# Kernel optimization log

Hardware: AMD Instinct MI355X
Metric: run time of the kernel (lower is better)

Reference implementation:

```python
import jax, jax.numpy as jnp
import numpy as np

N_NODES = 100000
N_EDGES = 1600000
N_FEAT = 64
HIDDEN = 64
N_GRAPHS = 256


def setup_inputs() -> dict:
    key = jax.random.key(0)
    ks = jax.random.split(key, 8)
    x = jax.random.normal(ks[0], (N_NODES, N_FEAT), dtype=jnp.float32)
    edge_index = jax.random.randint(ks[1], (2, N_EDGES), 0, N_NODES, dtype=jnp.int64)
    batch = jnp.sort(jax.random.randint(ks[2], (N_NODES,), 0, N_GRAPHS, dtype=jnp.int64))
    W1 = jax.random.normal(ks[3], (N_FEAT, HIDDEN), dtype=jnp.float32) / np.sqrt(N_FEAT)
    b1 = jnp.zeros((HIDDEN,), dtype=jnp.float32)
    W2 = jax.random.normal(ks[4], (HIDDEN, HIDDEN), dtype=jnp.float32) / np.sqrt(HIDDEN)
    b2 = jnp.zeros((HIDDEN,), dtype=jnp.float32)
    Wfc = jax.random.normal(ks[5], (HIDDEN, 1), dtype=jnp.float32) / np.sqrt(HIDDEN)
    bfc = jnp.zeros((1,), dtype=jnp.float32)
    return {"x": x, "edge_index": edge_index, "batch": batch,
            "W1": W1, "b1": b1, "W2": W2, "b2": b2, "Wfc": Wfc, "bfc": bfc}


def _gcn_conv(x, W, b, src, dst, norm, n_nodes):
    # h = X W, then symmetric-normalized scatter-add aggregation at dst
    h = x @ W  # [N, H]
    msg = h[src] * norm[:, None]  # [E+N, H] gather + scale
    agg = jax.ops.segment_sum(msg, dst, num_segments=n_nodes)
    return agg + b


def reference(x, edge_index, batch, W1, b1, W2, b2, Wfc, bfc):
    n = x.shape[0]
    loops = jnp.arange(n, dtype=edge_index.dtype)
    src = jnp.concatenate([edge_index[0], loops])  # add self-loops (GCNConv default)
    dst = jnp.concatenate([edge_index[1], loops])
    deg = jax.ops.segment_sum(jnp.ones_like(dst, dtype=x.dtype), dst, num_segments=n)
    dinv = jnp.where(deg > 0, jax.lax.rsqrt(deg), 0.0)
    norm = dinv[src] * dinv[dst]  # D^-1/2 (A+I) D^-1/2

    h = jax.nn.relu(_gcn_conv(x, W1, b1, src, dst, norm, n))  # dropout = identity (eval)
    h = jax.nn.relu(_gcn_conv(h, W2, b2, src, dst, norm, n))

    # global mean pool over graphs
    sums = jax.ops.segment_sum(h, batch, num_segments=N_GRAPHS)
    counts = jax.ops.segment_sum(jnp.ones((n,), dtype=h.dtype), batch, num_segments=N_GRAPHS)
    pooled = sums / jnp.maximum(counts, 1.0)[:, None]  # [G, H]
    return jax.nn.sigmoid(pooled @ Wfc + bfc)  # [G, 1]
```

## Files before the change

### kernel.cpp

```cpp
#include <hip/hip_runtime.h>
#include <hip/hip_fp16.h>
#include <math.h>

#define N_NODES  100000
#define N_EDGES  1600000
#define NF       64
#define N_GRAPHS 256

#define BSH   7
#define NB    ((N_NODES + 127) / 128)
#define BCAP  2600

typedef float f32x2 __attribute__((ext_vector_type(2)));

__global__ void k_zerocur(int* __restrict__ bucketCur) {
    int i = blockIdx.x * blockDim.x + threadIdx.x;
    if (i < NB) bucketCur[i] = 0;
}

__global__ __launch_bounds__(1024) void k_bscatter(const int* __restrict__ src,
                                                   const int* __restrict__ dst,
                                                   int* __restrict__ bucketCur,
                                                   int* __restrict__ scratch) {
    __shared__ int hist[NB];
    __shared__ int bbase[NB];
    int t = threadIdx.x;
    for (int i = t; i < NB; i += 1024) hist[i] = 0;
    __syncthreads();
    int e0 = (blockIdx.x * 1024 + t) * 8;
    int d[8], s[8], r[8];
    bool act = (e0 + 7) < N_EDGES;
    if (act) {
        *(int4*)&d[0] = *(const int4*)(dst + e0);
        *(int4*)&d[4] = *(const int4*)(dst + e0 + 4);
        *(int4*)&s[0] = *(const int4*)(src + e0);
        *(int4*)&s[4] = *(const int4*)(src + e0 + 4);
#pragma unroll
        for (int k = 0; k < 8; ++k) r[k] = atomicAdd(&hist[d[k] >> BSH], 1);
    }
    __syncthreads();
    for (int i = t; i < NB; i += 1024)
        if (hist[i]) bbase[i] = atomicAdd(&bucketCur[i], hist[i]);
    __syncthreads();
    if (act) {
#pragma unroll
        for (int k = 0; k < 8; ++k) {
            int b = d[k] >> BSH;
            int pos = bbase[b] + r[k];
            if (pos < BCAP)
                scratch[b * BCAP + pos] = ((d[k] & 127) << 17) | s[k];
        }
    }
}

__global__ __launch_bounds__(1024) void k_bscan(const int* __restrict__ bucketCur,
                                                int* __restrict__ bucketPtr,
                                                int* __restrict__ rowptr) {
    int t = threadIdx.x;
    __shared__ int ps[1024];
    int v = (t < NB) ? min(bucketCur[t], BCAP) : 0;
    ps[t] = v;
    __syncthreads();
#pragma unroll
    for (int off = 1; off < 1024; off <<= 1) {
        int u = (t >= off) ? ps[t - off] : 0;
        __syncthreads();
        ps[t] += u;
        __syncthreads();
    }
    if (t < NB) bucketPtr[t] = ps[t] - v;
    if (t == NB - 1) {
        bucketPtr[NB] = ps[t];
        rowptr[N_NODES] = ps[t];
    }
}

__global__ __launch_bounds__(256) void k_bfinal(const int* __restrict__ bucketCur,
                                                const int* __restrict__ bucketPtr,
                                                const int* __restrict__ scratch,
                                                int* __restrict__ rowptr,
                                                float* __restrict__ dinv,
                                                int* __restrict__ col) {
    int b = blockIdx.x;
    int cnt  = min(bucketCur[b], BCAP);
    int base = bucketPtr[b];
    int node0 = b << BSH;
    __shared__ int hist[128];
    __shared__ int escan[128];
    __shared__ int ps[128];
    __shared__ int rnk[BCAP];
    int t = threadIdx.x;
    if (t < 128) hist[t] = 0;
    __syncthreads();
    const int* sp = scratch + b * BCAP;
    for (int j = t; j < cnt; j += 256)
        rnk[j] = atomicAdd(&hist[sp[j] >> 17], 1);
    __syncthreads();
    int hv = (t < 128) ? hist[t] : 0;
    if (t < 128) ps[t] = hv;
    __syncthreads();
#pragma unroll
    for (int off = 1; off < 128; off <<= 1) {
        int u = 0;
        if (t < 128 && t >= off) u = ps[t - off];
        __syncthreads();
        if (t < 128) ps[t] += u;
        __syncthreads();
    }
    if (t < 128) {
        int excl = ps[t] - hv;
        escan[t] = excl;
        int node = node0 + t;
        if (node < N_NODES) {
            rowptr[node] = base + excl;
            dinv[node] = rsqrtf((float)(hv + 1));
        }
    }
    __syncthreads();
    for (int j = t; j < cnt; j += 256) {
        int pk = sp[j];
        col[base + escan[pk >> 17] + rnk[j]] = pk & 0x1FFFF;
    }
}

__global__ __launch_bounds__(256) void k_gemm(const float* __restrict__ X,
                                              const float* __restrict__ W,
                                              const float* __restrict__ bias,
                                              const float* __restrict__ dinv,
                                              int* __restrict__ Ah8) {
    __shared__ float Ws[64][64];
    __shared__ float Xs[64][68];
    int t  = threadIdx.x;
    int n0 = blockIdx.x * 64;

    for (int i = t; i < 64 * 64; i += 256) Ws[i >> 6][i & 63] = W[i];

#pragma unroll
    for (int p = 0; p < 4; ++p) {
        int flat = p * 256 + t;
        int nl = flat >> 4;
        int kg = flat & 15;
        int node = n0 + nl;
        float4 v = make_float4(0.f, 0.f, 0.f, 0.f);
        if (node < N_NODES) {
            v = *(const float4*)(X + (size_t)node * NF + kg * 4);
            if (bias) {
                v.x += bias[kg * 4 + 0]; v.x = v.x > 0.f ? v.x : 0.f;
                v.y += bias[kg * 4 + 1]; v.y = v.y > 0.f ? v.y : 0.f;
                v.z += bias[kg * 4 + 2]; v.z = v.z > 0.f ? v.z : 0.f;
                v.w += bias[kg * 4 + 3]; v.w = v.w > 0.f ? v.w : 0.f;
            }
        }
        Xs[kg * 4 + 0][nl] = v.x;
        Xs[kg * 4 + 1][nl] = v.y;
        Xs[kg * 4 + 2][nl] = v.z;
        Xs[kg * 4 + 3][nl] = v.w;
    }
    __syncthreads();

    int tx = t & 15;
    int ty = t >> 4;
    float acc[4][4];
#pragma unroll
    for (int i = 0; i < 4; ++i)
#pragma unroll
        for (int j = 0; j < 4; ++j) acc[i][j] = 0.f;

#pragma unroll 8
    for (int k = 0; k < 64; ++k) {
        float4 wv = *(const float4*)&Ws[k][tx * 4];
        float4 xv = *(const float4*)&Xs[k][ty * 4];
        acc[0][0] += xv.x * wv.x; acc[0][1] += xv.x * wv.y;
        acc[0][2] += xv.x * wv.z; acc[0][3] += xv.x * wv.w;
        acc[1][0] += xv.y * wv.x; acc[1][1] += xv.y * wv.y;
        acc[1][2] += xv.y * wv.z; acc[1][3] += xv.y * wv.w;
        acc[2][0] += xv.z * wv.x; acc[2][1] += xv.z * wv.y;
        acc[2][2] += xv.z * wv.z; acc[2][3] += xv.z * wv.w;
        acc[3][0] += xv.w * wv.x; acc[3][1] += xv.w * wv.y;
        acc[3][2] += xv.w * wv.z; acc[3][3] += xv.w * wv.w;
    }

#pragma unroll
    for (int i = 0; i < 4; ++i) {
        int node = n0 + ty * 4 + i;
        if (node < N_NODES) {
            float dv = dinv[node];
            int pk = 0;
            pk = __builtin_amdgcn_cvt_pk_fp8_f32(acc[i][0] * dv, acc[i][1] * dv, pk, false);
            pk = __builtin_amdgcn_cvt_pk_fp8_f32(acc[i][2] * dv, acc[i][3] * dv, pk, true);
            Ah8[(size_t)node * 16 + tx] = pk;
        }
    }
}

__global__ __launch_bounds__(256) void k_pull(const int* __restrict__ rowptr,
                                              const int* __restrict__ col,
                                              const float* __restrict__ dinv,
                                              const int* __restrict__ Ah8,
                                              float* __restrict__ B) {
    int n    = (blockIdx.x * blockDim.x + threadIdx.x) >> 6;
    int lane = threadIdx.x & 63;
    if (n >= N_NODES) return;
    int slot = lane >> 3;
    int oct  = lane & 7;
    int beg = rowptr[n];
    int cnt = rowptr[n + 1] - beg + 1;

    float acc0 = 0.f, acc1 = 0.f, acc2 = 0.f, acc3 = 0.f;
    float acc4 = 0.f, acc5 = 0.f, acc6 = 0.f, acc7 = 0.f;

    for (int base = slot; base < cnt; base += 32) {
        int cidx[4];
#pragma unroll
        for (int p = 0; p < 4; ++p) {
            int idx = base + p * 8;
            cidx[p] = (idx < cnt) ? ((idx == 0) ? n : col[beg + idx - 1]) : -1;
        }
#pragma unroll
        for (int p = 0; p < 4; ++p) {
            int s = cidx[p];
            if (s >= 0) {
                int2 raw = *(const int2*)(Ah8 + (size_t)s * 16 + oct * 2);
                f32x2 f0 = __builtin_amdgcn_cvt_pk_f32_fp8(raw.x, false);
                f32x2 f1 = __builtin_amdgcn_cvt_pk_f32_fp8(raw.x, true);
                f32x2 f2 = __builtin_amdgcn_cvt_pk_f32_fp8(raw.y, false);
                f32x2 f3 = __builtin_amdgcn_cvt_pk_f32_fp8(raw.y, true);
                acc0 += f0.x; acc1 += f0.y;
                acc2 += f1.x; acc3 += f1.y;
                acc4 += f2.x; acc5 += f2.y;
                acc6 += f3.x; acc7 += f3.y;
            }
        }
    }
#pragma unroll
    for (int off = 8; off < 64; off <<= 1) {
        acc0 += __shfl_down(acc0, off);
        acc1 += __shfl_down(acc1, off);
        acc2 += __shfl_down(acc2, off);
        acc3 += __shfl_down(acc3, off);
        acc4 += __shfl_down(acc4, off);
        acc5 += __shfl_down(acc5, off);
        acc6 += __shfl_down(acc6, off);
        acc7 += __shfl_down(acc7, off);
    }
    if (slot == 0) {
        float dv = dinv[n];
        float4 o0 = make_float4(acc0 * dv, acc1 * dv, acc2 * dv, acc3 * dv);
        float4 o1 = make_float4(acc4 * dv, acc5 * dv, acc6 * dv, acc7 * dv);
        *(float4*)(B + (size_t)n * NF + oct * 8)     = o0;
        *(float4*)(B + (size_t)n * NF + oct * 8 + 4) = o1;
    }
}

__device__ __forceinline__ int lower_bound_i(const int* __restrict__ a, int n, int key) {
    int lo = 0, hi = n;
    while (lo < hi) {
        int mid = (lo + hi) >> 1;
        if (a[mid] < key) lo = mid + 1; else hi = mid;
    }
    return lo;
}

__global__ __launch_bounds__(512) void k_pool_final(const float* __restrict__ B,
                                                    const int* __restrict__ batch,
                                                    const float* __restrict__ b2,
                                                    const float* __restrict__ Wfc,
                                                    const float* __restrict__ bfc,
                                                    float* __restrict__ out) {
    int g = blockIdx.x;
    __shared__ int s_lo, s_hi;
    int t = threadIdx.x;
    if (t == 0) {
        s_lo = lower_bound_i(batch, N_NODES, g);
        s_hi = lower_bound_i(batch, N_NODES, g + 1);
    }
    __syncthreads();
    int lo = s_lo, hi = s_hi;
    int ln = t >> 6, lane = t & 63;
    float bias = b2[lane];
    float acc = 0.0f;
    for (int n = lo + ln; n < hi; n += 8) {
        float v = B[(size_t)n * NF + lane] + bias;
        acc += v > 0.0f ? v : 0.0f;
    }
    __shared__ float red[8][64];
    red[ln][lane] = acc;
    __syncthreads();
    if (ln == 0) {
        float tot = 0.0f;
#pragma unroll
        for (int w = 0; w < 8; ++w) tot += red[w][lane];
        int cnt = hi - lo;
        float c = cnt > 0 ? (float)cnt : 1.0f;
        float v = (tot / c) * Wfc[lane];
#pragma unroll
        for (int off = 32; off > 0; off >>= 1) v += __shfl_down(v, off);
        if (lane == 0) out[g] = 1.0f / (1.0f + expf(-(v + bfc[0])));
    }
}

extern "C" void kernel_launch(void* const* d_in, const int* in_sizes, int n_in,
                              void* d_out, int out_size, void* d_ws, size_t ws_size,
                              hipStream_t stream) {
    const float* x    = (const float*)d_in[0];
    const int*   ei   = (const int*)d_in[1];
    const int*   batch= (const int*)d_in[2];
    const float* W1   = (const float*)d_in[3];
    const float* b1   = (const float*)d_in[4];
    const float* W2   = (const float*)d_in[5];
    const float* b2   = (const float*)d_in[6];
    const float* Wfc  = (const float*)d_in[7];
    const float* bfc  = (const float*)d_in[8];
    float* out = (float*)d_out;

    const int* src = ei;
    const int* dst = ei + N_EDGES;

    float*  B         = (float*)d_ws;
    int*    Ah8       = (int*)(B + (size_t)N_NODES * NF);
    float*  dinv      = (float*)(Ah8 + (size_t)N_NODES * 16);
    int*    rowptr    = (int*)(dinv + N_NODES);
    int*    bucketCur = rowptr + N_NODES + 1;
    int*    bucketPtr = bucketCur + NB;
    int*    col       = bucketPtr + NB + 1;
    int*    scratch   = col + N_EDGES;

    const int BLK = 256;
    int g_gemm  = (N_NODES + 63) / 64;
    int g_nwave = (N_NODES + 3) / 4;
    int g_bsc   = (N_EDGES / 8 + 1023) / 1024;

    k_zerocur<<<(NB + BLK - 1) / BLK, BLK, 0, stream>>>(bucketCur);
    k_bscatter<<<g_bsc, 1024, 0, stream>>>(src, dst, bucketCur, scratch);
    k_bscan<<<1, 1024, 0, stream>>>(bucketCur, bucketPtr, rowptr);
    k_bfinal<<<NB, BLK, 0, stream>>>(bucketCur, bucketPtr, scratch, rowptr, dinv, col);

    k_gemm<<<g_gemm, BLK, 0, stream>>>(x, W1, nullptr, dinv, Ah8);
    k_pull<<<g_nwave, BLK, 0, stream>>>(rowptr, col, dinv, Ah8, B);

    k_gemm<<<g_gemm, BLK, 0, stream>>>(B, W2, b1, dinv, Ah8);
    k_pull<<<g_nwave, BLK, 0, stream>>>(rowptr, col, dinv, Ah8, B);

    k_pool_final<<<N_GRAPHS, 512, 0, stream>>>(B, batch, b2, Wfc, bfc, out);
}
```

Baseline: 262.0 us.

## Fuse aggregation with GEMM and pooling, split fp8 features into halves

The layer-1 aggregation is fused into the layer-2 GEMM kernel and the layer-2 aggregation is fused with mean pooling, so the fp32 intermediate buffer B is never written or read. FP8 feature rows are split into two 32-byte half arrays, gathered in two passes with 16 edge slots per wave, to shrink the gather working set. Pooling accumulates per-block partial sums in shared memory and flushes them with global atomics. A small head kernel finishes the output. The cost is that each block now processes nodes one at a time per wave with a serial loop over 16 nodes and two passes. That may reduce parallelism and latency hiding compared with the previous one-wave-per-node pull.

```diff
diff --git a/kernel.cpp b/kernel.cpp
--- a/kernel.cpp
+++ b/kernel.cpp
@@ -1,5 +1,4 @@
 #include <hip/hip_runtime.h>
-#include <hip/hip_fp16.h>
 #include <math.h>
 
 #define N_NODES  100000
@@ -10,12 +9,14 @@
 #define BSH   7
 #define NB    ((N_NODES + 127) / 128)
 #define BCAP  2600
+#define NBLKS ((N_NODES + 63) / 64)
 
 typedef float f32x2 __attribute__((ext_vector_type(2)));
 
-__global__ void k_zerocur(int* __restrict__ bucketCur) {
+__global__ void k_zeroinit(int* __restrict__ bucketCur, float* __restrict__ gsums) {
     int i = blockIdx.x * blockDim.x + threadIdx.x;
     if (i < NB) bucketCur[i] = 0;
+    if (i < N_GRAPHS * NF) gsums[i] = 0.0f;
 }
 
 __global__ __launch_bounds__(1024) void k_bscatter(const int* __restrict__ src,
@@ -123,11 +124,11 @@
     }
 }
 
-__global__ __launch_bounds__(256) void k_gemm(const float* __restrict__ X,
-                                              const float* __restrict__ W,
-                                              const float* __restrict__ bias,
-                                              const float* __restrict__ dinv,
-                                              int* __restrict__ Ah8) {
+__global__ __launch_bounds__(256) void k_gemm1(const float* __restrict__ X,
+                                               const float* __restrict__ W,
+                                               const float* __restrict__ dinv,
+                                               int* __restrict__ A1a,
+                                               int* __restrict__ A1b) {
     __shared__ float Ws[64][64];
     __shared__ float Xs[64][68];
     int t  = threadIdx.x;
@@ -142,15 +143,7 @@
         int kg = flat & 15;
         int node = n0 + nl;
         float4 v = make_float4(0.f, 0.f, 0.f, 0.f);
-        if (node < N_NODES) {
-            v = *(const float4*)(X + (size_t)node * NF + kg * 4);
-            if (bias) {
-                v.x += bias[kg * 4 + 0]; v.x = v.x > 0.f ? v.x : 0.f;
-                v.y += bias[kg * 4 + 1]; v.y = v.y > 0.f ? v.y : 0.f;
-                v.z += bias[kg * 4 + 2]; v.z = v.z > 0.f ? v.z : 0.f;
-                v.w += bias[kg * 4 + 3]; v.w = v.w > 0.f ? v.w : 0.f;
-            }
-        }
+        if (node < N_NODES) v = *(const float4*)(X + (size_t)node * NF + kg * 4);
         Xs[kg * 4 + 0][nl] = v.x;
         Xs[kg * 4 + 1][nl] = v.y;
         Xs[kg * 4 + 2][nl] = v.z;
@@ -188,67 +181,170 @@
             int pk = 0;
             pk = __builtin_amdgcn_cvt_pk_fp8_f32(acc[i][0] * dv, acc[i][1] * dv, pk, false);
             pk = __builtin_amdgcn_cvt_pk_fp8_f32(acc[i][2] * dv, acc[i][3] * dv, pk, true);
-            Ah8[(size_t)node * 16 + tx] = pk;
-        }
-    }
-}
-
-__global__ __launch_bounds__(256) void k_pull(const int* __restrict__ rowptr,
-                                              const int* __restrict__ col,
-                                              const float* __restrict__ dinv,
-                                              const int* __restrict__ Ah8,
-                                              float* __restrict__ B) {
-    int n    = (blockIdx.x * blockDim.x + threadIdx.x) >> 6;
-    int lane = threadIdx.x & 63;
-    if (n >= N_NODES) return;
-    int slot = lane >> 3;
-    int oct  = lane & 7;
-    int beg = rowptr[n];
-    int cnt = rowptr[n + 1] - beg + 1;
-
-    float acc0 = 0.f, acc1 = 0.f, acc2 = 0.f, acc3 = 0.f;
-    float acc4 = 0.f, acc5 = 0.f, acc6 = 0.f, acc7 = 0.f;
-
-    for (int base = slot; base < cnt; base += 32) {
+            if (tx < 8) __builtin_nontemporal_store(pk, &A1a[(size_t)node * 8 + tx]);
+            else        __builtin_nontemporal_store(pk, &A1b[(size_t)node * 8 + tx - 8]);
+        }
+    }
+}
+
+__device__ __forceinline__ void pull_half(const int* __restrict__ A,
+                                          const int* __restrict__ col,
+                                          int n, int beg, int cnt,
+                                          int slot, int quad, float acc[8]) {
+#pragma unroll
+    for (int k = 0; k < 8; ++k) acc[k] = 0.f;
+    for (int base = slot; base < cnt; base += 64) {
         int cidx[4];
 #pragma unroll
         for (int p = 0; p < 4; ++p) {
-            int idx = base + p * 8;
+            int idx = base + p * 16;
             cidx[p] = (idx < cnt) ? ((idx == 0) ? n : col[beg + idx - 1]) : -1;
         }
 #pragma unroll
         for (int p = 0; p < 4; ++p) {
             int s = cidx[p];
             if (s >= 0) {
-                int2 raw = *(const int2*)(Ah8 + (size_t)s * 16 + oct * 2);
+                int2 raw = *(const int2*)(A + (size_t)s * 8 + quad * 2);
                 f32x2 f0 = __builtin_amdgcn_cvt_pk_f32_fp8(raw.x, false);
                 f32x2 f1 = __builtin_amdgcn_cvt_pk_f32_fp8(raw.x, true);
                 f32x2 f2 = __builtin_amdgcn_cvt_pk_f32_fp8(raw.y, false);
                 f32x2 f3 = __builtin_amdgcn_cvt_pk_f32_fp8(raw.y, true);
-                acc0 += f0.x; acc1 += f0.y;
-                acc2 += f1.x; acc3 += f1.y;
-                acc4 += f2.x; acc5 += f2.y;
-                acc6 += f3.x; acc7 += f3.y;
+                acc[0] += f0.x; acc[1] += f0.y; acc[2] += f1.x; acc[3] += f1.y;
+                acc[4] += f2.x; acc[5] += f2.y; acc[6] += f3.x; acc[7] += f3.y;
             }
         }
     }
 #pragma unroll
-    for (int off = 8; off < 64; off <<= 1) {
-        acc0 += __shfl_down(acc0, off);
-        acc1 += __shfl_down(acc1, off);
-        acc2 += __shfl_down(acc2, off);
-        acc3 += __shfl_down(acc3, off);
-        acc4 += __shfl_down(acc4, off);
-        acc5 += __shfl_down(acc5, off);
-        acc6 += __shfl_down(acc6, off);
-        acc7 += __shfl_down(acc7, off);
-    }
-    if (slot == 0) {
-        float dv = dinv[n];
-        float4 o0 = make_float4(acc0 * dv, acc1 * dv, acc2 * dv, acc3 * dv);
-        float4 o1 = make_float4(acc4 * dv, acc5 * dv, acc6 * dv, acc7 * dv);
-        *(float4*)(B + (size_t)n * NF + oct * 8)     = o0;
-        *(float4*)(B + (size_t)n * NF + oct * 8 + 4) = o1;
+    for (int off = 4; off < 64; off <<= 1)
+#pragma unroll
+        for (int k = 0; k < 8; ++k) acc[k] += __shfl_down(acc[k], off);
+}
+
+__global__ __launch_bounds__(256) void k_layer2(const int* __restrict__ rowptr,
+                                                const int* __restrict__ col,
+                                                const float* __restrict__ dinv,
+                                                const int* __restrict__ A1a,
+                                                const int* __restrict__ A1b,
+                                                const float* __restrict__ b1,
+                                                const float* __restrict__ W2,
+                                                int* __restrict__ A2a,
+                                                int* __restrict__ A2b) {
+    __shared__ float Ws[64][64];
+    __shared__ float Xs[64][68];
+    int t = threadIdx.x;
+    int n0 = blockIdx.x * 64;
+    for (int i = t; i < 64 * 64; i += 256) Ws[i >> 6][i & 63] = W2[i];
+    int wid = t >> 6, lane = t & 63, slot = lane >> 2, quad = lane & 3;
+
+    for (int h = 0; h < 2; ++h) {
+        const int* A = h ? A1b : A1a;
+        for (int i = 0; i < 16; ++i) {
+            int nl = wid * 16 + i;
+            int n = n0 + nl;
+            int fb = h * 32 + quad * 8;
+            if (n < N_NODES) {
+                int beg = rowptr[n];
+                int cnt = rowptr[n + 1] - beg + 1;
+                float acc[8];
+                pull_half(A, col, n, beg, cnt, slot, quad, acc);
+                if (slot == 0) {
+                    float dv = dinv[n];
+#pragma unroll
+                    for (int k = 0; k < 8; ++k) {
+                        float v = acc[k] * dv + b1[fb + k];
+                        Xs[fb + k][nl] = v > 0.f ? v : 0.f;
+                    }
+                }
+            } else if (slot == 0) {
+#pragma unroll
+                for (int k = 0; k < 8; ++k) Xs[fb + k][nl] = 0.f;
+            }
+        }
+    }
+    __syncthreads();
+
+    int tx = t & 15, ty = t >> 4;
+    float acc[4][4];
+#pragma unroll
+    for (int i = 0; i < 4; ++i)
+#pragma unroll
+        for (int j = 0; j < 4; ++j) acc[i][j] = 0.f;
+
+#pragma unroll 8
+    for (int k = 0; k < 64; ++k) {
+        float4 wv = *(const float4*)&Ws[k][tx * 4];
+        float4 xv = *(const float4*)&Xs[k][ty * 4];
+        acc[0][0] += xv.x * wv.x; acc[0][1] += xv.x * wv.y;
+        acc[0][2] += xv.x * wv.z; acc[0][3] += xv.x * wv.w;
+        acc[1][0] += xv.y * wv.x; acc[1][1] += xv.y * wv.y;
+        acc[1][2] += xv.y * wv.z; acc[1][3] += xv.y * wv.w;
+        acc[2][0] += xv.z * wv.x; acc[2][1] += xv.z * wv.y;
+        acc[2][2] += xv.z * wv.z; acc[2][3] += xv.z * wv.w;
+        acc[3][0] += xv.w * wv.x; acc[3][1] += xv.w * wv.y;
+        acc[3][2] += xv.w * wv.z; acc[3][3] += xv.w * wv.w;
+    }
+
+#pragma unroll
+    for (int i = 0; i < 4; ++i) {
+        int node = n0 + ty * 4 + i;
+        if (node < N_NODES) {
+            float dv = dinv[node];
+            int pk = 0;
+            pk = __builtin_amdgcn_cvt_pk_fp8_f32(acc[i][0] * dv, acc[i][1] * dv, pk, false);
+            pk = __builtin_amdgcn_cvt_pk_fp8_f32(acc[i][2] * dv, acc[i][3] * dv, pk, true);
+            if (tx < 8) __builtin_nontemporal_store(pk, &A2a[(size_t)node * 8 + tx]);
+            else        __builtin_nontemporal_store(pk, &A2b[(size_t)node * 8 + tx - 8]);
+        }
+    }
+}
+
+__global__ __launch_bounds__(256) void k_pool2(const int* __restrict__ rowptr,
+                                               const int* __restrict__ col,
+                                               const float* __restrict__ dinv,
+                                               const int* __restrict__ A2a,
+                                               const int* __restrict__ A2b,
+                                               const float* __restrict__ b2,
+                                               const int* __restrict__ batch,
+                                               float* __restrict__ gsums) {
+    __shared__ float gs[8][64];
+    __shared__ int sgmin;
+    int t = threadIdx.x;
+    int n0 = blockIdx.x * 64;
+    if (t == 0) sgmin = batch[n0];
+    for (int i = t; i < 8 * 64; i += 256) gs[i >> 6][i & 63] = 0.f;
+    __syncthreads();
+    int gmin = sgmin;
+    int wid = t >> 6, lane = t & 63, slot = lane >> 2, quad = lane & 3;
+
+    for (int h = 0; h < 2; ++h) {
+        const int* A = h ? A2b : A2a;
+        for (int i = 0; i < 16; ++i) {
+            int nl = wid * 16 + i;
+            int n = n0 + nl;
+            if (n >= N_NODES) continue;
+            int beg = rowptr[n];
+            int cnt = rowptr[n + 1] - beg + 1;
+            float acc[8];
+            pull_half(A, col, n, beg, cnt, slot, quad, acc);
+            if (slot == 0) {
+                float dv = dinv[n];
+                int g = batch[n];
+                int li = g - gmin;
+                int fb = h * 32 + quad * 8;
+#pragma unroll
+                for (int k = 0; k < 8; ++k) {
+                    float v = acc[k] * dv + b2[fb + k];
+                    v = v > 0.f ? v : 0.f;
+                    if (li < 8) atomicAdd(&gs[li][fb + k], v);
+                    else        atomicAdd(&gsums[g * NF + fb + k], v);
+                }
+            }
+        }
+    }
+    __syncthreads();
+    for (int j = t; j < 8 * 64; j += 256) {
+        float v = gs[j >> 6][j & 63];
+        if (v != 0.f) atomicAdd(&gsums[(gmin + (j >> 6)) * NF + (j & 63)], v);
     }
 }
 
@@ -261,42 +357,22 @@
     return lo;
 }
 
-__global__ __launch_bounds__(512) void k_pool_final(const float* __restrict__ B,
-                                                    const int* __restrict__ batch,
-                                                    const float* __restrict__ b2,
-                                                    const float* __restrict__ Wfc,
-                                                    const float* __restrict__ bfc,
-                                                    float* __restrict__ out) {
-    int g = blockIdx.x;
-    __shared__ int s_lo, s_hi;
-    int t = threadIdx.x;
-    if (t == 0) {
-        s_lo = lower_bound_i(batch, N_NODES, g);
-        s_hi = lower_bound_i(batch, N_NODES, g + 1);
-    }
-    __syncthreads();
-    int lo = s_lo, hi = s_hi;
-    int ln = t >> 6, lane = t & 63;
-    float bias = b2[lane];
-    float acc = 0.0f;
-    for (int n = lo + ln; n < hi; n += 8) {
-        float v = B[(size_t)n * NF + lane] + bias;
-        acc += v > 0.0f ? v : 0.0f;
-    }
-    __shared__ float red[8][64];
-    red[ln][lane] = acc;
-    __syncthreads();
-    if (ln == 0) {
-        float tot = 0.0f;
-#pragma unroll
-        for (int w = 0; w < 8; ++w) tot += red[w][lane];
-        int cnt = hi - lo;
-        float c = cnt > 0 ? (float)cnt : 1.0f;
-        float v = (tot / c) * Wfc[lane];
-#pragma unroll
-        for (int off = 32; off > 0; off >>= 1) v += __shfl_down(v, off);
-        if (lane == 0) out[g] = 1.0f / (1.0f + expf(-(v + bfc[0])));
-    }
+__global__ __launch_bounds__(256) void k_head(const float* __restrict__ gsums,
+                                              const int* __restrict__ batch,
+                                              const float* __restrict__ Wfc,
+                                              const float* __restrict__ bfc,
+                                              float* __restrict__ out) {
+    int g    = (blockIdx.x * blockDim.x + threadIdx.x) >> 6;
+    int lane = threadIdx.x & 63;
+    if (g >= N_GRAPHS) return;
+    int lo = lower_bound_i(batch, N_NODES, g);
+    int hi = lower_bound_i(batch, N_NODES, g + 1);
+    int cnt = hi - lo;
+    float c = cnt > 0 ? (float)cnt : 1.0f;
+    float v = (gsums[g * NF + lane] / c) * Wfc[lane];
+#pragma unroll
+    for (int off = 32; off > 0; off >>= 1) v += __shfl_down(v, off);
+    if (lane == 0) out[g] = 1.0f / (1.0f + expf(-(v + bfc[0])));
 }
 
 extern "C" void kernel_launch(void* const* d_in, const int* in_sizes, int n_in,
@@ -316,30 +392,30 @@
     const int* src = ei;
     const int* dst = ei + N_EDGES;
 
-    float*  B         = (float*)d_ws;
-    int*    Ah8       = (int*)(B + (size_t)N_NODES * NF);
-    float*  dinv      = (float*)(Ah8 + (size_t)N_NODES * 16);
-    int*    rowptr    = (int*)(dinv + N_NODES);
-    int*    bucketCur = rowptr + N_NODES + 1;
-    int*    bucketPtr = bucketCur + NB;
-    int*    col       = bucketPtr + NB + 1;
-    int*    scratch   = col + N_EDGES;
-
-    const int BLK = 256;
-    int g_gemm  = (N_NODES + 63) / 64;
-    int g_nwave = (N_NODES + 3) / 4;
-    int g_bsc   = (N_EDGES / 8 + 1023) / 1024;
-
-    k_zerocur<<<(NB + BLK - 1) / BLK, BLK, 0, stream>>>(bucketCur);
+    int*   A1a       = (int*)d_ws;
+    int*   A1b       = A1a + (size_t)N_NODES * 8;
+    int*   A2a       = A1b + (size_t)N_NODES * 8;
+    int*   A2b       = A2a + (size_t)N_NODES * 8;
+    float* dinv      = (float*)(A2b + (size_t)N_NODES * 8);
+    int*   rowptr    = (int*)(dinv + N_NODES);
+    int*   bucketCur = rowptr + N_NODES + 1;
+    int*   bucketPtr = bucketCur + NB;
+    float* gsums     = (float*)(bucketPtr + NB + 1);
+    int*   col       = (int*)(gsums + N_GRAPHS * NF);
+    int*   scratch   = col + N_EDGES;
+
+    int g_bsc = (N_EDGES / 8 + 1023) / 1024;
+
+    k_zeroinit<<<64, 256, 0, stream>>>(bucketCur, gsums);
     k_bscatter<<<g_bsc, 1024, 0, stream>>>(src, dst, bucketCur, scratch);
     k_bscan<<<1, 1024, 0, stream>>>(bucketCur, bucketPtr, rowptr);
-    k_bfinal<<<NB, BLK, 0, stream>>>(bucketCur, bucketPtr, scratch, rowptr, dinv, col);
-
-    k_gemm<<<g_gemm, BLK, 0, stream>>>(x, W1, nullptr, dinv, Ah8);
-    k_pull<<<g_nwave, BLK, 0, stream>>>(rowptr, col, dinv, Ah8, B);
-
-    k_gemm<<<g_gemm, BLK, 0, stream>>>(B, W2, b1, dinv, Ah8);
-    k_pull<<<g_nwave, BLK, 0, stream>>>(rowptr, col, dinv, Ah8, B);
-
-    k_pool_final<<<N_GRAPHS, 512, 0, stream>>>(B, batch, b2, Wfc, bfc, out);
-}
+    k_bfinal<<<NB, 256, 0, stream>>>(bucketCur, bucketPtr, scratch, rowptr, dinv, col);
+
+    k_gemm1<<<NBLKS, 256, 0, stream>>>(x, W1, dinv, A1a, A1b);
+
+    k_layer2<<<NBLKS, 256, 0, stream>>>(rowptr, col, dinv, A1a, A1b, b1, W2, A2a, A2b);
+
+    k_pool2<<<NBLKS, 256, 0, stream>>>(rowptr, col, dinv, A2a, A2b, b2, batch, gsums);
+
+    k_head<<<64, 256, 0, stream>>>(gsums, batch, Wfc, bfc, out);
+}
```

Result: slower. 418.9 us (+59.9%).

## Split fp8 feature table into two half-width arrays and gather each half separately

Applied to the files above, without the earlier changes.

The GEMM now writes the fp8 node features as two separate 32-byte-per-node arrays (first and second 32 features) instead of one 64-byte row. The pull kernel runs two passes, each gathering 8 bytes per lane from a half array, with 16 edge slots per wavefront instead of 8. The aim is to shrink the footprint of each gather pass so it caches better and to raise edge-level parallelism per wave. The cost is reading the column indices twice and doing two reductions, and each random gather now fetches only 32 bytes, which may waste cache-line bandwidth.

```diff
diff --git a/kernel.cpp b/kernel.cpp
--- a/kernel.cpp
+++ b/kernel.cpp
@@ -1,5 +1,4 @@
 #include <hip/hip_runtime.h>
-#include <hip/hip_fp16.h>
 #include <math.h>
 
 #define N_NODES  100000
@@ -10,6 +9,7 @@
 #define BSH   7
 #define NB    ((N_NODES + 127) / 128)
 #define BCAP  2600
+#define NBLKS ((N_NODES + 63) / 64)
 
 typedef float f32x2 __attribute__((ext_vector_type(2)));
 
@@ -127,7 +127,8 @@
                                               const float* __restrict__ W,
                                               const float* __restrict__ bias,
                                               const float* __restrict__ dinv,
-                                              int* __restrict__ Ah8) {
+                                              int* __restrict__ Aa,
+                                              int* __restrict__ Ab) {
     __shared__ float Ws[64][64];
     __shared__ float Xs[64][68];
     int t  = threadIdx.x;
@@ -188,7 +189,8 @@
             int pk = 0;
             pk = __builtin_amdgcn_cvt_pk_fp8_f32(acc[i][0] * dv, acc[i][1] * dv, pk, false);
             pk = __builtin_amdgcn_cvt_pk_fp8_f32(acc[i][2] * dv, acc[i][3] * dv, pk, true);
-            Ah8[(size_t)node * 16 + tx] = pk;
+            if (tx < 8) Aa[(size_t)node * 8 + tx] = pk;
+            else        Ab[(size_t)node * 8 + tx - 8] = pk;
         }
     }
 }
@@ -196,59 +198,57 @@
 __global__ __launch_bounds__(256) void k_pull(const int* __restrict__ rowptr,
                                               const int* __restrict__ col,
                                               const float* __restrict__ dinv,
-                                              const int* __restrict__ Ah8,
+                                              const int* __restrict__ Aa,
+                                              const int* __restrict__ Ab,
                                               float* __restrict__ B) {
     int n    = (blockIdx.x * blockDim.x + threadIdx.x) >> 6;
     int lane = threadIdx.x & 63;
     if (n >= N_NODES) return;
-    int slot = lane >> 3;
-    int oct  = lane & 7;
+    int slot = lane >> 2;
+    int quad = lane & 3;
     int beg = rowptr[n];
     int cnt = rowptr[n + 1] - beg + 1;
-
-    float acc0 = 0.f, acc1 = 0.f, acc2 = 0.f, acc3 = 0.f;
-    float acc4 = 0.f, acc5 = 0.f, acc6 = 0.f, acc7 = 0.f;
-
-    for (int base = slot; base < cnt; base += 32) {
-        int cidx[4];
-#pragma unroll
-        for (int p = 0; p < 4; ++p) {
-            int idx = base + p * 8;
-            cidx[p] = (idx < cnt) ? ((idx == 0) ? n : col[beg + idx - 1]) : -1;
-        }
-#pragma unroll
-        for (int p = 0; p < 4; ++p) {
-            int s = cidx[p];
-            if (s >= 0) {
-                int2 raw = *(const int2*)(Ah8 + (size_t)s * 16 + oct * 2);
-                f32x2 f0 = __builtin_amdgcn_cvt_pk_f32_fp8(raw.x, false);
-                f32x2 f1 = __builtin_amdgcn_cvt_pk_f32_fp8(raw.x, true);
-                f32x2 f2 = __builtin_amdgcn_cvt_pk_f32_fp8(raw.y, false);
-                f32x2 f3 = __builtin_amdgcn_cvt_pk_f32_fp8(raw.y, true);
-                acc0 += f0.x; acc1 += f0.y;
-                acc2 += f1.x; acc3 += f1.y;
-                acc4 += f2.x; acc5 += f2.y;
-                acc6 += f3.x; acc7 += f3.y;
+    float dv = dinv[n];
+
+#pragma unroll
+    for (int h = 0; h < 2; ++h) {
+        const int* __restrict__ A = h ? Ab : Aa;
+        float acc[8];
+#pragma unroll
+        for (int k = 0; k < 8; ++k) acc[k] = 0.f;
+
+        for (int base = slot; base < cnt; base += 64) {
+            int cidx[4];
+#pragma unroll
+            for (int p = 0; p < 4; ++p) {
+                int idx = base + p * 16;
+                cidx[p] = (idx < cnt) ? ((idx == 0) ? n : col[beg + idx - 1]) : -1;
             }
-        }
-    }
-#pragma unroll
-    for (int off = 8; off < 64; off <<= 1) {
-        acc0 += __shfl_down(acc0, off);
-        acc1 += __shfl_down(acc1, off);
-        acc2 += __shfl_down(acc2, off);
-        acc3 += __shfl_down(acc3, off);
-        acc4 += __shfl_down(acc4, off);
-        acc5 += __shfl_down(acc5, off);
-        acc6 += __shfl_down(acc6, off);
-        acc7 += __shfl_down(acc7, off);
-    }
-    if (slot == 0) {
-        float dv = dinv[n];
-        float4 o0 = make_float4(acc0 * dv, acc1 * dv, acc2 * dv, acc3 * dv);
-        float4 o1 = make_float4(acc4 * dv, acc5 * dv, acc6 * dv, acc7 * dv);
-        *(float4*)(B + (size_t)n * NF + oct * 8)     = o0;
-        *(float4*)(B + (size_t)n * NF + oct * 8 + 4) = o1;
+#pragma unroll
+            for (int p = 0; p < 4; ++p) {
+                int s = cidx[p];
+                if (s >= 0) {
+                    int2 raw = *(const int2*)(A + (size_t)s * 8 + quad * 2);
+                    f32x2 f0 = __builtin_amdgcn_cvt_pk_f32_fp8(raw.x, false);
+                    f32x2 f1 = __builtin_amdgcn_cvt_pk_f32_fp8(raw.x, true);
+                    f32x2 f2 = __builtin_amdgcn_cvt_pk_f32_fp8(raw.y, false);
+                    f32x2 f3 = __builtin_amdgcn_cvt_pk_f32_fp8(raw.y, true);
+                    acc[0] += f0.x; acc[1] += f0.y; acc[2] += f1.x; acc[3] += f1.y;
+                    acc[4] += f2.x; acc[5] += f2.y; acc[6] += f3.x; acc[7] += f3.y;
+                }
+            }
+        }
+#pragma unroll
+        for (int off = 4; off < 64; off <<= 1)
+#pragma unroll
+            for (int k = 0; k < 8; ++k) acc[k] += __shfl_down(acc[k], off);
+
+        if (slot == 0) {
+            float4 o0 = make_float4(acc[0] * dv, acc[1] * dv, acc[2] * dv, acc[3] * dv);
+            float4 o1 = make_float4(acc[4] * dv, acc[5] * dv, acc[6] * dv, acc[7] * dv);
+            *(float4*)(B + (size_t)n * NF + h * 32 + quad * 8)     = o0;
+            *(float4*)(B + (size_t)n * NF + h * 32 + quad * 8 + 4) = o1;
+        }
     }
 }
 
@@ -316,17 +316,17 @@
     const int* src = ei;
     const int* dst = ei + N_EDGES;
 
-    float*  B         = (float*)d_ws;
-    int*    Ah8       = (int*)(B + (size_t)N_NODES * NF);
-    float*  dinv      = (float*)(Ah8 + (size_t)N_NODES * 16);
-    int*    rowptr    = (int*)(dinv + N_NODES);
-    int*    bucketCur = rowptr + N_NODES + 1;
-    int*    bucketPtr = bucketCur + NB;
-    int*    col       = bucketPtr + NB + 1;
-    int*    scratch   = col + N_EDGES;
+    float* B         = (float*)d_ws;
+    int*   Aa        = (int*)(B + (size_t)N_NODES * NF);
+    int*   Ab        = Aa + (size_t)N_NODES * 8;
+    float* dinv      = (float*)(Ab + (size_t)N_NODES * 8);
+    int*   rowptr    = (int*)(dinv + N_NODES);
+    int*   bucketCur = rowptr + N_NODES + 1;
+    int*   bucketPtr = bucketCur + NB;
+    int*   col       = bucketPtr + NB + 1;
+    int*   scratch   = col + N_EDGES;
 
     const int BLK = 256;
-    int g_gemm  = (N_NODES + 63) / 64;
     int g_nwave = (N_NODES + 3) / 4;
     int g_bsc   = (N_EDGES / 8 + 1023) / 1024;
 
@@ -335,11 +335,11 @@
     k_bscan<<<1, 1024, 0, stream>>>(bucketCur, bucketPtr, rowptr);
     k_bfinal<<<NB, BLK, 0, stream>>>(bucketCur, bucketPtr, scratch, rowptr, dinv, col);
 
-    k_gemm<<<g_gemm, BLK, 0, stream>>>(x, W1, nullptr, dinv, Ah8);
-    k_pull<<<g_nwave, BLK, 0, stream>>>(rowptr, col, dinv, Ah8, B);
-
-    k_gemm<<<g_gemm, BLK, 0, stream>>>(B, W2, b1, dinv, Ah8);
-    k_pull<<<g_nwave, BLK, 0, stream>>>(rowptr, col, dinv, Ah8, B);
+    k_gemm<<<NBLKS, BLK, 0, stream>>>(x, W1, nullptr, dinv, Aa, Ab);
+    k_pull<<<g_nwave, BLK, 0, stream>>>(rowptr, col, dinv, Aa, Ab, B);
+
+    k_gemm<<<NBLKS, BLK, 0, stream>>>(B, W2, b1, dinv, Aa, Ab);
+    k_pull<<<g_nwave, BLK, 0, stream>>>(rowptr, col, dinv, Aa, Ab, B);
 
     k_pool_final<<<N_GRAPHS, 512, 0, stream>>>(B, batch, b2, Wfc, bfc, out);
 }
```

Measured after the change: 312.3 us. 19.2% more time.
